# Kernel tuning notes

Hardware: AMD Instinct MI355X
Metric: run time of the kernel (lower is better)

## Reference

```python
import jax, jax.numpy as jnp
import numpy as np

ALPHA = 0.1
K = 2

def setup_inputs() -> dict:
    key = jax.random.key(0)
    ks = jax.random.split(key, 8)
    N, E, IN, OUT, NQ = 50000, 800000, 512, 128, 100000
    return {
        "x": jax.random.normal(ks[0], (N, IN), dtype=jnp.float32),
        "edge_index": jax.random.randint(ks[1], (2, E), 0, N, dtype=jnp.int64),
        "q_emb": jax.random.normal(ks[2], (NQ, IN), dtype=jnp.float32),
        "W_t": jax.random.normal(ks[3], (IN, OUT), dtype=jnp.float32) * (IN ** -0.5),
        "b_t": jax.random.normal(ks[4], (OUT,), dtype=jnp.float32) * 0.01,
        "W_q": jax.random.normal(ks[5], (IN, OUT), dtype=jnp.float32) * (IN ** -0.5),
        "b_q": jax.random.normal(ks[6], (OUT,), dtype=jnp.float32) * 0.01,
    }

def appnp(h0, edge_index, num_nodes):
    # GCN normalization with self-loops: D^{-1/2}(A+I)D^{-1/2}
    loops = jnp.arange(num_nodes, dtype=edge_index.dtype)
    row = jnp.concatenate([edge_index[0], loops])  # source
    col = jnp.concatenate([edge_index[1], loops])  # target
    deg = jax.ops.segment_sum(jnp.ones(col.shape, dtype=h0.dtype), col, num_segments=num_nodes)
    dinv = jnp.where(deg > 0, jax.lax.rsqrt(jnp.maximum(deg, 1e-12)), 0.0)
    norm = dinv[row] * dinv[col]  # [E+N]
    h = h0
    for _ in range(K):
        msg = norm[:, None] * h[row]                                  # [E+N, d]
        agg = jax.ops.segment_sum(msg, col, num_segments=num_nodes)   # [N, d]
        h = (1.0 - ALPHA) * agg + ALPHA * h0
    return h

def reference(x, edge_index, q_emb, W_t, b_t, W_q, b_q):
    # dropout layers are identity in eval mode
    h0 = x @ W_t + b_t                 # t_encoder: [N, out]
    h = appnp(h0, edge_index, x.shape[0])
    ques = q_emb @ W_q + b_q           # q_encoder: [NQ, out]
    return (ques, h)
```

## Files before the change

### kernel.cpp

```cpp
#include <hip/hip_runtime.h>
#include <hip/hip_bf16.h>

#define IN_DIM 512
#define OUT_DIM 128

#define BIDX(k, c) ((k)*144 + (c) + (((c) >> 5) << 2))

__global__ __launch_bounds__(256) void gemm_dual_kernel(
    const float* __restrict__ A0, const float* __restrict__ W0,
    const float* __restrict__ b0, float* __restrict__ C0, int M0, int nb0,
    const float* __restrict__ A1, const float* __restrict__ W1,
    const float* __restrict__ b1, float* __restrict__ C1, int M1)
{
    __shared__ float At[16][128];
    __shared__ float BtF[16 * 144];

    const float* A; const float* W; const float* bias; float* C; int M, bid;
    if ((int)blockIdx.x < nb0) {
        A = A0; W = W0; bias = b0; C = C0; M = M0; bid = blockIdx.x;
    } else {
        A = A1; W = W1; bias = b1; C = C1; M = M1; bid = blockIdx.x - nb0;
    }

    const int tid  = threadIdx.x;
    const int row0 = bid * 128;
    const int rg = tid >> 4;
    const int cg = tid & 15;
    const int r0 = rg * 8;
    const int c0 = cg * 8;

    float acc[8][8];
#pragma unroll
    for (int i = 0; i < 8; ++i)
#pragma unroll
        for (int j = 0; j < 8; ++j) acc[i][j] = 0.0f;

    const int ra = tid >> 1;
    const int ka = (tid & 1) * 8;
    int arow = row0 + ra;
    if (arow > M - 1) arow = M - 1;
    const float* aptr = A + (size_t)arow * IN_DIM + ka;

    const int kb = tid >> 4;
    const int cb = (tid & 15) * 8;
    const float* wptr = W + (size_t)kb * OUT_DIM + cb;

    for (int kk = 0; kk < IN_DIM; kk += 16) {
        const float4 a0 = *(const float4*)(aptr + kk);
        const float4 a1 = *(const float4*)(aptr + kk + 4);
        const float4 b0v = *(const float4*)(wptr + (size_t)kk * OUT_DIM);
        const float4 b1v = *(const float4*)(wptr + (size_t)kk * OUT_DIM + 4);
        __syncthreads();
        At[ka + 0][ra] = a0.x; At[ka + 1][ra] = a0.y;
        At[ka + 2][ra] = a0.z; At[ka + 3][ra] = a0.w;
        At[ka + 4][ra] = a1.x; At[ka + 5][ra] = a1.y;
        At[ka + 6][ra] = a1.z; At[ka + 7][ra] = a1.w;
        *(float4*)&BtF[BIDX(kb, cb)]     = b0v;
        *(float4*)&BtF[BIDX(kb, cb) + 4] = b1v;
        __syncthreads();
#pragma unroll
        for (int k = 0; k < 16; ++k) {
            const float4 av0 = *(const float4*)&At[k][r0];
            const float4 av1 = *(const float4*)&At[k][r0 + 4];
            const float4 bv0 = *(const float4*)&BtF[BIDX(k, c0)];
            const float4 bv1 = *(const float4*)&BtF[BIDX(k, c0) + 4];
            const float ar[8] = {av0.x, av0.y, av0.z, av0.w,
                                 av1.x, av1.y, av1.z, av1.w};
            const float bc[8] = {bv0.x, bv0.y, bv0.z, bv0.w,
                                 bv1.x, bv1.y, bv1.z, bv1.w};
#pragma unroll
            for (int i = 0; i < 8; ++i)
#pragma unroll
                for (int j = 0; j < 8; ++j)
                    acc[i][j] = fmaf(ar[i], bc[j], acc[i][j]);
        }
    }

    const float4 bb0 = *(const float4*)(bias + c0);
    const float4 bb1 = *(const float4*)(bias + c0 + 4);
#pragma unroll
    for (int i = 0; i < 8; ++i) {
        const int r = row0 + r0 + i;
        if (r < M) {
            float4 o0 = make_float4(acc[i][0] + bb0.x, acc[i][1] + bb0.y,
                                    acc[i][2] + bb0.z, acc[i][3] + bb0.w);
            float4 o1 = make_float4(acc[i][4] + bb1.x, acc[i][5] + bb1.y,
                                    acc[i][6] + bb1.z, acc[i][7] + bb1.w);
            *(float4*)(C + (size_t)r * OUT_DIM + c0)     = o0;
            *(float4*)(C + (size_t)r * OUT_DIM + c0 + 4) = o1;
        }
    }
}

__global__ void count_kernel(const int* __restrict__ col, int* __restrict__ cnt,
                             int E)
{
    for (int e = blockIdx.x * blockDim.x + threadIdx.x; e < E;
         e += gridDim.x * blockDim.x)
        atomicAdd(&cnt[col[e]], 1);
}

__global__ void dinv_kernel(const int* __restrict__ cnt,
                            float* __restrict__ dinv, int N)
{
    int n = blockIdx.x * blockDim.x + threadIdx.x;
    if (n < N) dinv[n] = rsqrtf((float)cnt[n] + 1.0f);
}

__global__ __launch_bounds__(1024) void scan_kernel(
    const int* __restrict__ cnt, int* __restrict__ off, int* __restrict__ cur,
    int N)
{
    __shared__ int buf[1024];
    const int tid   = threadIdx.x;
    const int chunk = (N + 1023) / 1024;
    const int lo    = tid * chunk;
    const int hi    = min(N, lo + chunk);

    int total = 0;
    for (int i = lo; i < hi; ++i) total += cnt[i];
    buf[tid] = total;
    __syncthreads();
#pragma unroll
    for (int ofs = 1; ofs < 1024; ofs <<= 1) {
        const int t = (tid >= ofs) ? buf[tid - ofs] : 0;
        __syncthreads();
        buf[tid] += t;
        __syncthreads();
    }
    int running = buf[tid] - total;
    for (int i = lo; i < hi; ++i) {
        off[i] = running;
        cur[i] = running;
        running += cnt[i];
    }
    if (tid == 1023) off[N] = running;
}

__global__ void fill_kernel(const int* __restrict__ row,
                            const int* __restrict__ col,
                            const float* __restrict__ dinv,
                            int* __restrict__ cur, int* __restrict__ csr_row,
                            float* __restrict__ csr_w, int E)
{
    for (int e = blockIdx.x * blockDim.x + threadIdx.x; e < E;
         e += gridDim.x * blockDim.x) {
        const int c = col[e];
        const int r = row[e];
        const int p = atomicAdd(&cur[c], 1);
        csr_row[p] = r;
        csr_w[p]   = dinv[r];
    }
}

__global__ __launch_bounds__(256) void spmm_kernel(
    const float* __restrict__ hin, const float* __restrict__ h0,
    const float* __restrict__ dinv, const int* __restrict__ off,
    const int* __restrict__ csr_row, const float* __restrict__ csr_w,
    float* __restrict__ hout, int N)
{
    const int wave = threadIdx.x >> 6;
    const int lane = threadIdx.x & 63;
    const int n = blockIdx.x * 4 + wave;
    if (n >= N) return;
    const int f = lane * 2;

    float acc0 = 0.0f, acc1 = 0.0f;
    const int s = off[n];
    const int e = off[n + 1];

    int i = s;
    for (; i + 3 < e; i += 4) {
        const int   r0i = csr_row[i],     r1i = csr_row[i + 1];
        const int   r2i = csr_row[i + 2], r3i = csr_row[i + 3];
        const float w0 = csr_w[i],     w1 = csr_w[i + 1];
        const float w2 = csr_w[i + 2], w3 = csr_w[i + 3];
        const float2 v0 = *(const float2*)(hin + (size_t)r0i * OUT_DIM + f);
        const float2 v1 = *(const float2*)(hin + (size_t)r1i * OUT_DIM + f);
        const float2 v2 = *(const float2*)(hin + (size_t)r2i * OUT_DIM + f);
        const float2 v3 = *(const float2*)(hin + (size_t)r3i * OUT_DIM + f);
        acc0 = fmaf(w0, v0.x, fmaf(w1, v1.x, fmaf(w2, v2.x, fmaf(w3, v3.x, acc0))));
        acc1 = fmaf(w0, v0.y, fmaf(w1, v1.y, fmaf(w2, v2.y, fmaf(w3, v3.y, acc1))));
    }
    for (; i < e; ++i) {
        const int   r = csr_row[i];
        const float w = csr_w[i];
        const float2 v = *(const float2*)(hin + (size_t)r * OUT_DIM + f);
        acc0 = fmaf(w, v.x, acc0);
        acc1 = fmaf(w, v.y, acc1);
    }

    const float di  = dinv[n];
    const float2 hs  = *(const float2*)(hin + (size_t)n * OUT_DIM + f);
    const float2 h0v = *(const float2*)(h0  + (size_t)n * OUT_DIM + f);
    float2 o;
    o.x = 0.9f * (di * acc0 + di * di * hs.x) + 0.1f * h0v.x;
    o.y = 0.9f * (di * acc1 + di * di * hs.y) + 0.1f * h0v.y;
    *(float2*)(hout + (size_t)n * OUT_DIM + f) = o;
}

extern "C" void kernel_launch(void* const* d_in, const int* in_sizes, int n_in,
                              void* d_out, int out_size, void* d_ws,
                              size_t ws_size, hipStream_t stream)
{
    const float* x     = (const float*)d_in[0];
    const int*   ei    = (const int*)d_in[1];
    const float* q_emb = (const float*)d_in[2];
    const float* W_t   = (const float*)d_in[3];
    const float* b_t   = (const float*)d_in[4];
    const float* W_q   = (const float*)d_in[5];
    const float* b_q   = (const float*)d_in[6];

    const int OUT = in_sizes[4];
    const int IN  = in_sizes[3] / OUT;
    const int N   = in_sizes[0] / IN;
    const int E   = in_sizes[1] / 2;
    const int NQ  = in_sizes[2] / IN;

    const int* row = ei;
    const int* col = ei + E;

    char*  w   = (char*)d_ws;
    size_t ofs = 0;
    auto take = [&](size_t bytes) -> void* {
        void* p = w + ofs;
        ofs += (bytes + 255) & ~(size_t)255;
        return p;
    };
    float* h0    = (float*)take((size_t)N * OUT * 4);
    float* h1    = (float*)take((size_t)N * OUT * 4);
    float* dinv  = (float*)take((size_t)N * 4);
    int*   cnt   = (int*)take((size_t)N * 4);
    int*   offp  = (int*)take((size_t)(N + 1) * 4);
    int*   cur   = (int*)take((size_t)N * 4);
    int*   csr_r = (int*)take((size_t)E * 4);
    float* csr_w = (float*)take((size_t)E * 4);
    (void)ws_size; (void)n_in; (void)out_size;

    float* out_q = (float*)d_out;
    float* out_h = (float*)d_out + (size_t)NQ * OUT;

    hipMemsetAsync(cnt, 0, (size_t)N * 4, stream);

    const int nb_q = (NQ + 127) / 128;
    const int nb_t = (N + 127) / 128;
    gemm_dual_kernel<<<nb_q + nb_t, 256, 0, stream>>>(
        q_emb, W_q, b_q, out_q, NQ, nb_q,
        x,     W_t, b_t, h0,    N);

    count_kernel<<<1024, 256, 0, stream>>>(col, cnt, E);
    dinv_kernel<<<(N + 255) / 256, 256, 0, stream>>>(cnt, dinv, N);
    scan_kernel<<<1, 1024, 0, stream>>>(cnt, offp, cur, N);
    fill_kernel<<<1024, 256, 0, stream>>>(row, col, dinv, cur, csr_r, csr_w, E);

    spmm_kernel<<<(N + 3) / 4, 256, 0, stream>>>(h0, h0, dinv, offp, csr_r,
                                                 csr_w, h1, N);
    spmm_kernel<<<(N + 3) / 4, 256, 0, stream>>>(h1, h0, dinv, offp, csr_r,
                                                 csr_w, out_h, N);
}
```

Before: 822.5 us.

## Move dual GEMM onto bf16 MFMA with split-precision hi/lo emulation

```diff
diff --git a/kernel.cpp b/kernel.cpp
--- a/kernel.cpp
+++ b/kernel.cpp
@@ -4,90 +4,155 @@
 #define IN_DIM 512
 #define OUT_DIM 128
 
-#define BIDX(k, c) ((k)*144 + (c) + (((c) >> 5) << 2))
+typedef short bf16x8 __attribute__((ext_vector_type(8)));
+typedef float f32x4  __attribute__((ext_vector_type(4)));
+
+static __device__ __forceinline__ unsigned short f32_to_bf16_rne(float f) {
+    unsigned u = __builtin_bit_cast(unsigned, f);
+    unsigned r = u + 0x7FFFu + ((u >> 16) & 1u);
+    return (unsigned short)(r >> 16);
+}
+static __device__ __forceinline__ float bf16_bits_to_f32(unsigned short h) {
+    return __builtin_bit_cast(float, (unsigned)h << 16);
+}
+
+__global__ __launch_bounds__(256) void wtrans_kernel(
+    const float* __restrict__ W, short* __restrict__ Th, short* __restrict__ Tl)
+{
+    const int id = blockIdx.x * 256 + threadIdx.x;
+    const int k = id >> 7;
+    const int n = id & 127;
+    const float w = W[id];
+    const unsigned short hb = f32_to_bf16_rne(w);
+    const unsigned short lb = f32_to_bf16_rne(w - bf16_bits_to_f32(hb));
+    Th[n * 512 + k] = (short)hb;
+    Tl[n * 512 + k] = (short)lb;
+}
 
 __global__ __launch_bounds__(256) void gemm_dual_kernel(
-    const float* __restrict__ A0, const float* __restrict__ W0,
-    const float* __restrict__ b0, float* __restrict__ C0, int M0, int nb0,
-    const float* __restrict__ A1, const float* __restrict__ W1,
-    const float* __restrict__ b1, float* __restrict__ C1, int M1)
-{
-    __shared__ float At[16][128];
-    __shared__ float BtF[16 * 144];
-
-    const float* A; const float* W; const float* bias; float* C; int M, bid;
+    const float* __restrict__ A0, const short* __restrict__ Th0,
+    const short* __restrict__ Tl0, const float* __restrict__ b0,
+    float* __restrict__ C0, int M0, int nb0,
+    const float* __restrict__ A1, const short* __restrict__ Th1,
+    const short* __restrict__ Tl1, const float* __restrict__ b1,
+    float* __restrict__ C1, int M1)
+{
+    __shared__ short lAh[128 * 64];
+    __shared__ short lAl[128 * 64];
+    __shared__ short lBh[128 * 64];
+    __shared__ short lBl[128 * 64];
+
+    const float* A; const short* Th; const short* Tl; const float* bias;
+    float* C; int M, bid;
     if ((int)blockIdx.x < nb0) {
-        A = A0; W = W0; bias = b0; C = C0; M = M0; bid = blockIdx.x;
+        A = A0; Th = Th0; Tl = Tl0; bias = b0; C = C0; M = M0; bid = blockIdx.x;
     } else {
-        A = A1; W = W1; bias = b1; C = C1; M = M1; bid = blockIdx.x - nb0;
+        A = A1; Th = Th1; Tl = Tl1; bias = b1; C = C1; M = M1;
+        bid = blockIdx.x - nb0;
     }
 
     const int tid  = threadIdx.x;
-    const int row0 = bid * 128;
-    const int rg = tid >> 4;
-    const int cg = tid & 15;
-    const int r0 = rg * 8;
-    const int c0 = cg * 8;
-
-    float acc[8][8];
-#pragma unroll
-    for (int i = 0; i < 8; ++i)
-#pragma unroll
-        for (int j = 0; j < 8; ++j) acc[i][j] = 0.0f;
-
-    const int ra = tid >> 1;
-    const int ka = (tid & 1) * 8;
-    int arow = row0 + ra;
-    if (arow > M - 1) arow = M - 1;
-    const float* aptr = A + (size_t)arow * IN_DIM + ka;
-
-    const int kb = tid >> 4;
-    const int cb = (tid & 15) * 8;
-    const float* wptr = W + (size_t)kb * OUT_DIM + cb;
-
-    for (int kk = 0; kk < IN_DIM; kk += 16) {
-        const float4 a0 = *(const float4*)(aptr + kk);
-        const float4 a1 = *(const float4*)(aptr + kk + 4);
-        const float4 b0v = *(const float4*)(wptr + (size_t)kk * OUT_DIM);
-        const float4 b1v = *(const float4*)(wptr + (size_t)kk * OUT_DIM + 4);
+    const int lane = tid & 63;
+    const int wav  = tid >> 6;
+    const int wm   = wav >> 1;
+    const int wn   = wav & 1;
+    const int m0   = bid * 128;
+
+    f32x4 acc[4][4];
+#pragma unroll
+    for (int i = 0; i < 4; ++i)
+#pragma unroll
+        for (int j = 0; j < 4; ++j) acc[i][j] = (f32x4){0.f, 0.f, 0.f, 0.f};
+
+    const int sr = tid >> 3;
+    const int sg = tid & 7;
+
+    const int fr  = lane & 15;
+    const int fq  = lane >> 4;
+    const unsigned swz = (unsigned)((lane & 7) << 4);
+
+    for (int ks = 0; ks < IN_DIM; ks += 64) {
         __syncthreads();
-        At[ka + 0][ra] = a0.x; At[ka + 1][ra] = a0.y;
-        At[ka + 2][ra] = a0.z; At[ka + 3][ra] = a0.w;
-        At[ka + 4][ra] = a1.x; At[ka + 5][ra] = a1.y;
-        At[ka + 6][ra] = a1.z; At[ka + 7][ra] = a1.w;
-        *(float4*)&BtF[BIDX(kb, cb)]     = b0v;
-        *(float4*)&BtF[BIDX(kb, cb) + 4] = b1v;
+#pragma unroll
+        for (int it = 0; it < 4; ++it) {
+            const int r = it * 32 + sr;
+            int grow = m0 + r; if (grow > M - 1) grow = M - 1;
+            const float* p = A + (size_t)grow * IN_DIM + ks + sg * 8;
+            const float4 fa = *(const float4*)p;
+            const float4 fb = *(const float4*)(p + 4);
+            const float vals[8] = {fa.x, fa.y, fa.z, fa.w, fb.x, fb.y, fb.z, fb.w};
+            bf16x8 h8, l8;
+#pragma unroll
+            for (int j = 0; j < 8; ++j) {
+                const unsigned short hb = f32_to_bf16_rne(vals[j]);
+                const unsigned short lb =
+                    f32_to_bf16_rne(vals[j] - bf16_bits_to_f32(hb));
+                h8[j] = (short)hb; l8[j] = (short)lb;
+            }
+            const unsigned byte = (unsigned)(r * 128 + sg * 16) ^
+                                  (unsigned)((r & 7) << 4);
+            *(bf16x8*)((char*)lAh + byte) = h8;
+            *(bf16x8*)((char*)lAl + byte) = l8;
+        }
+#pragma unroll
+        for (int it = 0; it < 4; ++it) {
+            const int n = it * 32 + sr;
+            const size_t src = (size_t)n * IN_DIM + ks + sg * 8;
+            const bf16x8 h8 = *(const bf16x8*)(Th + src);
+            const bf16x8 l8 = *(const bf16x8*)(Tl + src);
+            const unsigned byte = (unsigned)(n * 128 + sg * 16) ^
+                                  (unsigned)((n & 7) << 4);
+            *(bf16x8*)((char*)lBh + byte) = h8;
+            *(bf16x8*)((char*)lBl + byte) = l8;
+        }
         __syncthreads();
-#pragma unroll
-        for (int k = 0; k < 16; ++k) {
-            const float4 av0 = *(const float4*)&At[k][r0];
-            const float4 av1 = *(const float4*)&At[k][r0 + 4];
-            const float4 bv0 = *(const float4*)&BtF[BIDX(k, c0)];
-            const float4 bv1 = *(const float4*)&BtF[BIDX(k, c0) + 4];
-            const float ar[8] = {av0.x, av0.y, av0.z, av0.w,
-                                 av1.x, av1.y, av1.z, av1.w};
-            const float bc[8] = {bv0.x, bv0.y, bv0.z, bv0.w,
-                                 bv1.x, bv1.y, bv1.z, bv1.w};
-#pragma unroll
-            for (int i = 0; i < 8; ++i)
-#pragma unroll
-                for (int j = 0; j < 8; ++j)
-                    acc[i][j] = fmaf(ar[i], bc[j], acc[i][j]);
-        }
-    }
-
-    const float4 bb0 = *(const float4*)(bias + c0);
-    const float4 bb1 = *(const float4*)(bias + c0 + 4);
-#pragma unroll
-    for (int i = 0; i < 8; ++i) {
-        const int r = row0 + r0 + i;
-        if (r < M) {
-            float4 o0 = make_float4(acc[i][0] + bb0.x, acc[i][1] + bb0.y,
-                                    acc[i][2] + bb0.z, acc[i][3] + bb0.w);
-            float4 o1 = make_float4(acc[i][4] + bb1.x, acc[i][5] + bb1.y,
-                                    acc[i][6] + bb1.z, acc[i][7] + bb1.w);
-            *(float4*)(C + (size_t)r * OUT_DIM + c0)     = o0;
-            *(float4*)(C + (size_t)r * OUT_DIM + c0 + 4) = o1;
+
+#pragma unroll
+        for (int kk = 0; kk < 2; ++kk) {
+            const unsigned cb = (unsigned)(kk * 64 + fq * 16);
+            bf16x8 ah[4], al[4], bh[4], bl[4];
+#pragma unroll
+            for (int mt = 0; mt < 4; ++mt) {
+                const int r = wm * 64 + mt * 16 + fr;
+                const unsigned byte = ((unsigned)(r * 128) + cb) ^ swz;
+                ah[mt] = *(const bf16x8*)((const char*)lAh + byte);
+                al[mt] = *(const bf16x8*)((const char*)lAl + byte);
+            }
+#pragma unroll
+            for (int nt = 0; nt < 4; ++nt) {
+                const int n = wn * 64 + nt * 16 + fr;
+                const unsigned byte = ((unsigned)(n * 128) + cb) ^ swz;
+                bh[nt] = *(const bf16x8*)((const char*)lBh + byte);
+                bl[nt] = *(const bf16x8*)((const char*)lBl + byte);
+            }
+#pragma unroll
+            for (int mt = 0; mt < 4; ++mt)
+#pragma unroll
+                for (int nt = 0; nt < 4; ++nt) {
+                    acc[mt][nt] = __builtin_amdgcn_mfma_f32_16x16x32_bf16(
+                        ah[mt], bh[nt], acc[mt][nt], 0, 0, 0);
+                    acc[mt][nt] = __builtin_amdgcn_mfma_f32_16x16x32_bf16(
+                        ah[mt], bl[nt], acc[mt][nt], 0, 0, 0);
+                    acc[mt][nt] = __builtin_amdgcn_mfma_f32_16x16x32_bf16(
+                        al[mt], bh[nt], acc[mt][nt], 0, 0, 0);
+                }
+        }
+    }
+
+    float bv[4];
+#pragma unroll
+    for (int nt = 0; nt < 4; ++nt) bv[nt] = bias[wn * 64 + nt * 16 + fr];
+#pragma unroll
+    for (int mt = 0; mt < 4; ++mt) {
+#pragma unroll
+        for (int i = 0; i < 4; ++i) {
+            const int row = m0 + wm * 64 + mt * 16 + fq * 4 + i;
+            if (row < M) {
+                float* cp = C + (size_t)row * OUT_DIM + wn * 64 + fr;
+#pragma unroll
+                for (int nt = 0; nt < 4; ++nt)
+                    cp[nt * 16] = acc[mt][nt][i] + bv[nt];
+            }
         }
     }
 }
@@ -170,17 +235,18 @@
     const int e = off[n + 1];
 
     int i = s;
-    for (; i + 3 < e; i += 4) {
-        const int   r0i = csr_row[i],     r1i = csr_row[i + 1];
-        const int   r2i = csr_row[i + 2], r3i = csr_row[i + 3];
-        const float w0 = csr_w[i],     w1 = csr_w[i + 1];
-        const float w2 = csr_w[i + 2], w3 = csr_w[i + 3];
-        const float2 v0 = *(const float2*)(hin + (size_t)r0i * OUT_DIM + f);
-        const float2 v1 = *(const float2*)(hin + (size_t)r1i * OUT_DIM + f);
-        const float2 v2 = *(const float2*)(hin + (size_t)r2i * OUT_DIM + f);
-        const float2 v3 = *(const float2*)(hin + (size_t)r3i * OUT_DIM + f);
-        acc0 = fmaf(w0, v0.x, fmaf(w1, v1.x, fmaf(w2, v2.x, fmaf(w3, v3.x, acc0))));
-        acc1 = fmaf(w0, v0.y, fmaf(w1, v1.y, fmaf(w2, v2.y, fmaf(w3, v3.y, acc1))));
+    for (; i + 7 < e; i += 8) {
+        int   rr[8]; float ww[8]; float2 vv[8];
+#pragma unroll
+        for (int j = 0; j < 8; ++j) { rr[j] = csr_row[i + j]; ww[j] = csr_w[i + j]; }
+#pragma unroll
+        for (int j = 0; j < 8; ++j)
+            vv[j] = *(const float2*)(hin + (size_t)rr[j] * OUT_DIM + f);
+#pragma unroll
+        for (int j = 0; j < 8; ++j) {
+            acc0 = fmaf(ww[j], vv[j].x, acc0);
+            acc1 = fmaf(ww[j], vv[j].y, acc1);
+        }
     }
     for (; i < e; ++i) {
         const int   r = csr_row[i];
@@ -235,18 +301,25 @@
     int*   cur   = (int*)take((size_t)N * 4);
     int*   csr_r = (int*)take((size_t)E * 4);
     float* csr_w = (float*)take((size_t)E * 4);
+    short* Tq_h  = (short*)take((size_t)IN * OUT * 2);
+    short* Tq_l  = (short*)take((size_t)IN * OUT * 2);
+    short* Tt_h  = (short*)take((size_t)IN * OUT * 2);
+    short* Tt_l  = (short*)take((size_t)IN * OUT * 2);
     (void)ws_size; (void)n_in; (void)out_size;
 
     float* out_q = (float*)d_out;
     float* out_h = (float*)d_out + (size_t)NQ * OUT;
 
     hipMemsetAsync(cnt, 0, (size_t)N * 4, stream);
+
+    wtrans_kernel<<<256, 256, 0, stream>>>(W_q, Tq_h, Tq_l);
+    wtrans_kernel<<<256, 256, 0, stream>>>(W_t, Tt_h, Tt_l);
 
     const int nb_q = (NQ + 127) / 128;
     const int nb_t = (N + 127) / 128;
     gemm_dual_kernel<<<nb_q + nb_t, 256, 0, stream>>>(
-        q_emb, W_q, b_q, out_q, NQ, nb_q,
-        x,     W_t, b_t, h0,    N);
+        q_emb, Tq_h, Tq_l, b_q, out_q, NQ, nb_q,
+        x,     Tt_h, Tt_l, b_t, h0,    N);
 
     count_kernel<<<1024, 256, 0, stream>>>(col, cnt, E);
     dinv_kernel<<<(N + 255) / 256, 256, 0, stream>>>(cnt, dinv, N);
```

New measurement: 751.3 us. 8.7% less time.
